# Kernel tuning notes

Hardware: AMD Instinct MI355X
Metric: run time of the kernel (lower is better)

## Reference

```python
import jax, jax.numpy as jnp
import numpy as np

BLOCK = 32  # GGML Q8_0 block size


def setup_inputs() -> dict:
    key = jax.random.key(0)
    k1, k2, k3, k4 = jax.random.split(key, 4)
    B, S, I, O = 2, 2048, 4096, 16384
    x = jax.random.normal(k1, (B, S, I), dtype=jnp.float32)
    # Q8_0-style signed 8-bit quants stored as int32 for portability
    qweight = jax.random.randint(k2, (O, I), -127, 128, dtype=jnp.int32)
    # one positive fp scale per 32-element block
    scales = jax.random.uniform(k3, (O, I // BLOCK), dtype=jnp.float32,
                                minval=0.005, maxval=0.02)
    bias = jax.random.normal(k4, (O,), dtype=jnp.float32) * 0.01
    return {"x": x, "qweight": qweight, "scales": scales, "bias": bias}


def reference(x, qweight, scales, bias):
    # dequantize_tensor: per-block scale * int8 quants -> full precision weight
    O, I = qweight.shape
    w = qweight.astype(x.dtype).reshape(O, I // BLOCK, BLOCK) * scales[:, :, None]
    w = w.reshape(O, I)  # [O, I]
    # Linear forward: y = x @ W^T + b
    return jnp.einsum('bsd,od->bso', x, w) + bias
```

## Files before the change

kernel.cpp:

```cpp
#include <hip/hip_runtime.h>
#include <cstdint>
#include <cstddef>

#define M_DIM 4096
#define N_DIM 16384
#define K_DIM 4096
#define QBLK 32

typedef __bf16 bf16x8 __attribute__((ext_vector_type(8)));
typedef float  f32x4  __attribute__((ext_vector_type(4)));
typedef unsigned short u16x8 __attribute__((ext_vector_type(8)));

__device__ __forceinline__ unsigned short f2bf(float f) {
    unsigned int x = __builtin_bit_cast(unsigned int, f);
    x += 0x7fffu + ((x >> 16) & 1u);
    return (unsigned short)(x >> 16);
}

__device__ __forceinline__ void gload16(const void* g, void* l) {
    __builtin_amdgcn_global_load_lds((__attribute__((address_space(1))) unsigned int*)(g),
                                     (__attribute__((address_space(3))) unsigned int*)(l),
                                     16, 0, 0);
}

__global__ __launch_bounds__(256) void cvt_x_kernel(const float* __restrict__ x,
                                                    unsigned short* __restrict__ o) {
    const size_t total = (size_t)M_DIM * K_DIM / 8;
    for (size_t i = (size_t)blockIdx.x * 256 + threadIdx.x; i < total;
         i += (size_t)gridDim.x * 256) {
        const float4* src = (const float4*)(x + i * 8);
        float4 a0 = src[0], a1 = src[1];
        u16x8 v;
        v[0] = f2bf(a0.x); v[1] = f2bf(a0.y); v[2] = f2bf(a0.z); v[3] = f2bf(a0.w);
        v[4] = f2bf(a1.x); v[5] = f2bf(a1.y); v[6] = f2bf(a1.z); v[7] = f2bf(a1.w);
        *(u16x8*)(o + i * 8) = v;
    }
}

__global__ __launch_bounds__(256) void dequant_w_kernel(const int* __restrict__ q,
                                                        const float* __restrict__ s,
                                                        unsigned short* __restrict__ o) {
    const size_t total = (size_t)N_DIM * K_DIM / 8;
    for (size_t i = (size_t)blockIdx.x * 256 + threadIdx.x; i < total;
         i += (size_t)gridDim.x * 256) {
        const int4* src = (const int4*)(q + i * 8);
        int4 q0 = src[0], q1 = src[1];
        float sc = s[i >> 2];
        u16x8 v;
        v[0] = f2bf((float)q0.x * sc); v[1] = f2bf((float)q0.y * sc);
        v[2] = f2bf((float)q0.z * sc); v[3] = f2bf((float)q0.w * sc);
        v[4] = f2bf((float)q1.x * sc); v[5] = f2bf((float)q1.y * sc);
        v[6] = f2bf((float)q1.z * sc); v[7] = f2bf((float)q1.w * sc);
        *(u16x8*)(o + i * 8) = v;
    }
}

__global__ __launch_bounds__(512, 2) void gemm256(
    const unsigned short* __restrict__ Abf, const unsigned short* __restrict__ Bbf,
    const float* __restrict__ bias, float* __restrict__ out) {

    __shared__ char smem[131072];

    const int t  = threadIdx.x;
    const int l  = t & 63;
    const int w  = t >> 6;
    const int wm = w >> 2;
    const int wn = w & 3;

    const int bid = blockIdx.y * 64 + blockIdx.x;
    const int wg  = (bid & 7) * 128 + (bid >> 3);
    const int bx  = wg & 63;
    const int by  = wg >> 6;
    const int tileM = by * 256;
    const int tileN = bx * 256;

    const int sr = w * 8 + (l >> 3);
    const int cs = (l & 7) ^ (l >> 3);
    const char* aP = (const char*)Abf + (size_t)(tileM + sr) * (K_DIM * 2) + cs * 16;
    const char* bP = (const char*)Bbf + (size_t)(tileN + sr) * (K_DIM * 2) + cs * 16;
    const int wq = w * 1024;

    const int lrow = l & 15, l47 = l >> 4;
    const int sw = lrow & 7;
    const unsigned c0 = (unsigned)((l47 ^ sw) * 16);
    const unsigned c1 = (unsigned)(((4 + l47) ^ sw) * 16);
    const unsigned offA0 = (unsigned)((wm * 64 + lrow) * 128) + c0;
    const unsigned offA1 = (unsigned)((wm * 64 + lrow) * 128) + c1;
    const unsigned offB0 = (unsigned)((wn * 32 + lrow) * 128) + c0;
    const unsigned offB1 = (unsigned)((wn * 32 + lrow) * 128) + c1;

    bf16x8 avr[4][2];
    bf16x8 bvr[2][2][2];
    f32x4  acc[2][4][2][2] = {};

#define ST_A(H, KT, DB) do { \
    const char* g_ = aP + (size_t)(H) * 1048576u + (unsigned)(KT) * 128u; \
    char* d_ = smem + (DB) * 65536 + (H) * 16384 + wq; \
    gload16(g_, d_); gload16(g_ + 524288, d_ + 8192); } while (0)

#define ST_B(H, KT, DB) do { \
    const char* g_ = bP + (size_t)(H) * 1048576u + (unsigned)(KT) * 128u; \
    char* d_ = smem + (DB) * 65536 + 32768 + (H) * 16384 + wq; \
    gload16(g_, d_); gload16(g_ + 8192 * 64, d_ + 8192); } while (0)

#define RD_A(DB, MH) do { \
    const char* b_ = smem + (DB) * 65536 + (MH) * 16384; \
    _Pragma("unroll") for (int mf_ = 0; mf_ < 4; ++mf_) { \
        avr[mf_][0] = *(const bf16x8*)(b_ + offA0 + mf_ * 2048); \
        avr[mf_][1] = *(const bf16x8*)(b_ + offA1 + mf_ * 2048); } } while (0)

#define RD_B(DB, NH) do { \
    const char* b_ = smem + (DB) * 65536 + 32768 + (NH) * 16384; \
    _Pragma("unroll") for (int nf_ = 0; nf_ < 2; ++nf_) { \
        bvr[NH][nf_][0] = *(const bf16x8*)(b_ + offB0 + nf_ * 2048); \
        bvr[NH][nf_][1] = *(const bf16x8*)(b_ + offB1 + nf_ * 2048); } } while (0)

#define MMQ(MH, NH) do { __builtin_amdgcn_s_setprio(1); \
    _Pragma("unroll") for (int mf_ = 0; mf_ < 4; ++mf_) \
    _Pragma("unroll") for (int nf_ = 0; nf_ < 2; ++nf_) \
    _Pragma("unroll") for (int kk_ = 0; kk_ < 2; ++kk_) \
        acc[MH][mf_][NH][nf_] = __builtin_amdgcn_mfma_f32_16x16x32_bf16( \
            avr[mf_][kk_], bvr[NH][nf_][kk_], acc[MH][mf_][NH][nf_], 0, 0, 0); \
    __builtin_amdgcn_s_setprio(0); } while (0)

#define BAR __builtin_amdgcn_s_barrier()
#define LGKM do { asm volatile("s_waitcnt lgkmcnt(0)" ::: "memory"); \
                  __builtin_amdgcn_sched_barrier(0); } while (0)
#define VMC(N) asm volatile("s_waitcnt vmcnt(" #N ")" ::: "memory")

    ST_A(0, 0, 0); ST_A(1, 0, 0); ST_B(0, 0, 0); ST_B(1, 0, 0);
    ST_A(0, 1, 1); ST_B(0, 1, 1);
    VMC(4); BAR;

    for (int i = 0; i < 32; ++i) {
        const int k0 = 2 * i;
        const int ka = (k0 + 1) & 63;
        const int kb = (k0 + 2) & 63;
        const int kc = (k0 + 3) & 63;
        RD_A(0, 0); RD_B(0, 0); ST_A(1, ka, 1); BAR; LGKM; MMQ(0, 0); BAR;
        RD_B(0, 1);             ST_B(1, ka, 1); BAR; LGKM; MMQ(0, 1); BAR;
        RD_A(0, 1);             ST_A(0, kb, 0); BAR; LGKM; MMQ(1, 0); BAR;
                                ST_B(0, kb, 0); BAR;       MMQ(1, 1); VMC(4); BAR;
        RD_A(1, 0); RD_B(1, 0); ST_A(1, kb, 0); BAR; LGKM; MMQ(0, 0); BAR;
        RD_B(1, 1);             ST_B(1, kb, 0); BAR; LGKM; MMQ(0, 1); BAR;
        RD_A(1, 1);             ST_A(0, kc, 1); BAR; LGKM; MMQ(1, 0); BAR;
                                ST_B(0, kc, 1); BAR;       MMQ(1, 1); VMC(4); BAR;
    }

    VMC(0);

    #pragma unroll
    for (int mh = 0; mh < 2; ++mh)
    #pragma unroll
    for (int nh = 0; nh < 2; ++nh)
    #pragma unroll
    for (int nf = 0; nf < 2; ++nf) {
        const int col = tileN + nh * 128 + wn * 32 + nf * 16 + lrow;
        const float bv = bias[col];
        #pragma unroll
        for (int mf = 0; mf < 4; ++mf) {
            const int row0 = tileM + mh * 128 + wm * 64 + mf * 16 + l47 * 4;
            f32x4 v = acc[mh][mf][nh][nf];
            #pragma unroll
            for (int j = 0; j < 4; ++j)
                out[(size_t)(row0 + j) * N_DIM + col] = v[j] + bv;
        }
    }
#undef ST_A
#undef ST_B
#undef RD_A
#undef RD_B
#undef MMQ
#undef BAR
#undef LGKM
#undef VMC
}

__global__ __launch_bounds__(256, 2) void gemm_fused(
    const float* __restrict__ Xf, const int* __restrict__ Qw, const float* __restrict__ Sc,
    const float* __restrict__ bias, float* __restrict__ out) {

    __shared__ char smem[2 * 32768];
    const int t = threadIdx.x;
    const int l = t & 63;
    const int w = t >> 6;
    const int wm = w >> 1, wn = w & 1;
    const int rowA0 = blockIdx.y * 128;
    const int colB0 = blockIdx.x * 128;

    const int lr = l >> 3;
    const int sXor = (l & 7) ^ lr;

    const float* aSrcF[4]; const int* bSrcQ[4]; const float* bSrcS[4];
    #pragma unroll
    for (int j = 0; j < 4; ++j) {
        int c = w * 4 + j;
        aSrcF[j] = Xf + (size_t)(rowA0 + c * 8 + lr) * K_DIM + sXor * 8;
        bSrcQ[j] = Qw + (size_t)(colB0 + c * 8 + lr) * K_DIM + sXor * 8;
        bSrcS[j] = Sc + (size_t)(colB0 + c * 8 + lr) * (K_DIM / QBLK) + (sXor >> 2);
    }

    const int lrow = l & 15, l47 = l >> 4, lx = l & 7;
    const unsigned raB0 = (unsigned)((wm * 64 + lrow) * 128 + ((l47 ^ lx) * 16));
    const unsigned raB1 = (unsigned)((wm * 64 + lrow) * 128 + (((4 | l47) ^ lx) * 16));
    const unsigned rbB0 = (unsigned)(16384 + (wn * 64 + lrow) * 128 + ((l47 ^ lx) * 16));
    const unsigned rbB1 = (unsigned)(16384 + (wn * 64 + lrow) * 128 + (((4 | l47) ^ lx) * 16));

    float fA[4][8]; int qB[4][8]; float sB[4];
    auto load_s = [&]() {
        #pragma unroll
        for (int j = 0; j < 4; ++j) {
            float4 a0 = ((const float4*)aSrcF[j])[0];
            float4 a1 = ((const float4*)aSrcF[j])[1];
            fA[j][0] = a0.x; fA[j][1] = a0.y; fA[j][2] = a0.z; fA[j][3] = a0.w;
            fA[j][4] = a1.x; fA[j][5] = a1.y; fA[j][6] = a1.z; fA[j][7] = a1.w;
            aSrcF[j] += 64;
            int4 b0 = ((const int4*)bSrcQ[j])[0];
            int4 b1 = ((const int4*)bSrcQ[j])[1];
            qB[j][0] = b0.x; qB[j][1] = b0.y; qB[j][2] = b0.z; qB[j][3] = b0.w;
            qB[j][4] = b1.x; qB[j][5] = b1.y; qB[j][6] = b1.z; qB[j][7] = b1.w;
            bSrcQ[j] += 64;
            sB[j] = *bSrcS[j]; bSrcS[j] += 2;
        }
    };
    auto write_s = [&](int bsel) {
        #pragma unroll
        for (int j = 0; j < 4; ++j) {
            u16x8 va, vb;
            #pragma unroll
            for (int e = 0; e < 8; ++e) va[e] = f2bf(fA[j][e]);
            #pragma unroll
            for (int e = 0; e < 8; ++e) vb[e] = f2bf((float)qB[j][e] * sB[j]);
            *(u16x8*)(&smem[bsel * 32768 + (w * 4 + j) * 1024 + l * 16]) = va;
            *(u16x8*)(&smem[bsel * 32768 + 16384 + (w * 4 + j) * 1024 + l * 16]) = vb;
        }
    };

    f32x4 acc[4][4] = {};
    load_s(); write_s(0);
    __syncthreads();
    int bsel = 0;
    for (int kt = 0; kt < 64; ++kt) {
        const bool pre = (kt + 1 < 64);
        if (pre) load_s();
        const unsigned boff = (unsigned)(bsel * 32768);
        #pragma unroll
        for (int kk = 0; kk < 2; ++kk) {
            bf16x8 av[4], bv[4];
            const unsigned ra = (kk ? raB1 : raB0) + boff;
            const unsigned rb = (kk ? rbB1 : rbB0) + boff;
            #pragma unroll
            for (int mf = 0; mf < 4; ++mf) av[mf] = *(const bf16x8*)(&smem[ra + mf * 2048]);
            #pragma unroll
            for (int nf = 0; nf < 4; ++nf) bv[nf] = *(const bf16x8*)(&smem[rb + nf * 2048]);
            #pragma unroll
            for (int mf = 0; mf < 4; ++mf)
                #pragma unroll
                for (int nf = 0; nf < 4; ++nf)
                    acc[mf][nf] = __builtin_amdgcn_mfma_f32_16x16x32_bf16(
                        av[mf], bv[nf], acc[mf][nf], 0, 0, 0);
        }
        if (pre) write_s(bsel ^ 1);
        __syncthreads();
        bsel ^= 1;
    }
    const int orow0 = rowA0 + wm * 64 + l47 * 4;
    const int ocol0 = colB0 + wn * 64 + lrow;
    #pragma unroll
    for (int nf = 0; nf < 4; ++nf) {
        const float bv = bias[ocol0 + nf * 16];
        #pragma unroll
        for (int mf = 0; mf < 4; ++mf) {
            f32x4 v = acc[mf][nf];
            #pragma unroll
            for (int j = 0; j < 4; ++j)
                out[(size_t)(orow0 + mf * 16 + j) * N_DIM + (ocol0 + nf * 16)] = v[j] + bv;
        }
    }
}

extern "C" void kernel_launch(void* const* d_in, const int* in_sizes, int n_in,
                              void* d_out, int out_size, void* d_ws, size_t ws_size,
                              hipStream_t stream) {
    const float* x    = (const float*)d_in[0];
    const int*   qw   = (const int*)d_in[1];
    const float* sc   = (const float*)d_in[2];
    const float* bias = (const float*)d_in[3];
    float* out = (float*)d_out;

    const size_t need = ((size_t)M_DIM * K_DIM + (size_t)N_DIM * K_DIM) * 2;
    if (ws_size >= need) {
        unsigned short* xb = (unsigned short*)d_ws;
        unsigned short* wb = xb + (size_t)M_DIM * K_DIM;
        cvt_x_kernel<<<dim3(2048), dim3(256), 0, stream>>>(x, xb);
        dequant_w_kernel<<<dim3(4096), dim3(256), 0, stream>>>(qw, sc, wb);
        gemm256<<<dim3(64, 16), dim3(512), 0, stream>>>(xb, wb, bias, out);
    } else {
        gemm_fused<<<dim3(128, 32), dim3(256), 0, stream>>>(x, qw, sc, bias, out);
    }
}
```

Measured before the change: 923.7 us.

## Issue all LDS fragment reads up front and drop intermediate barriers per k-tile

Restructures the 256x256 bf16 GEMM main loop so each k-tile loads all four A/B fragment sets from LDS at once into separate register buffers. MFMA groups are then gated by partial lgkmcnt waits instead of full waits. Three of the four block barriers per quarter-step are removed, leaving two per tile. The goal is less barrier and LDS-latency stall between MFMA bursts, at the cost of more live VGPRs (two A and two B fragment buffers) and a changed ordering of global-to-LDS stores relative to reads.

```diff
diff --git a/kernel.cpp b/kernel.cpp
--- a/kernel.cpp
+++ b/kernel.cpp
@@ -89,8 +89,8 @@
     const unsigned offB0 = (unsigned)((wn * 32 + lrow) * 128) + c0;
     const unsigned offB1 = (unsigned)((wn * 32 + lrow) * 128) + c1;
 
-    bf16x8 avr[4][2];
-    bf16x8 bvr[2][2][2];
+    bf16x8 avr0[4][2], avr1[4][2];
+    bf16x8 bvr0[2][2], bvr1[2][2];
     f32x4  acc[2][4][2][2] = {};
 
 #define ST_A(H, KT, DB) do { \
@@ -101,50 +101,55 @@
 #define ST_B(H, KT, DB) do { \
     const char* g_ = bP + (size_t)(H) * 1048576u + (unsigned)(KT) * 128u; \
     char* d_ = smem + (DB) * 65536 + 32768 + (H) * 16384 + wq; \
-    gload16(g_, d_); gload16(g_ + 8192 * 64, d_ + 8192); } while (0)
-
-#define RD_A(DB, MH) do { \
+    gload16(g_, d_); gload16(g_ + 524288, d_ + 8192); } while (0)
+
+#define RD_A(DB, MH, DST) do { \
     const char* b_ = smem + (DB) * 65536 + (MH) * 16384; \
     _Pragma("unroll") for (int mf_ = 0; mf_ < 4; ++mf_) { \
-        avr[mf_][0] = *(const bf16x8*)(b_ + offA0 + mf_ * 2048); \
-        avr[mf_][1] = *(const bf16x8*)(b_ + offA1 + mf_ * 2048); } } while (0)
-
-#define RD_B(DB, NH) do { \
+        DST[mf_][0] = *(const bf16x8*)(b_ + offA0 + mf_ * 2048); \
+        DST[mf_][1] = *(const bf16x8*)(b_ + offA1 + mf_ * 2048); } } while (0)
+
+#define RD_B(DB, NH, DST) do { \
     const char* b_ = smem + (DB) * 65536 + 32768 + (NH) * 16384; \
     _Pragma("unroll") for (int nf_ = 0; nf_ < 2; ++nf_) { \
-        bvr[NH][nf_][0] = *(const bf16x8*)(b_ + offB0 + nf_ * 2048); \
-        bvr[NH][nf_][1] = *(const bf16x8*)(b_ + offB1 + nf_ * 2048); } } while (0)
-
-#define MMQ(MH, NH) do { __builtin_amdgcn_s_setprio(1); \
+        DST[nf_][0] = *(const bf16x8*)(b_ + offB0 + nf_ * 2048); \
+        DST[nf_][1] = *(const bf16x8*)(b_ + offB1 + nf_ * 2048); } } while (0)
+
+#define MMQ(MH, NH, AV, BV) do { __builtin_amdgcn_s_setprio(1); \
     _Pragma("unroll") for (int mf_ = 0; mf_ < 4; ++mf_) \
     _Pragma("unroll") for (int nf_ = 0; nf_ < 2; ++nf_) \
     _Pragma("unroll") for (int kk_ = 0; kk_ < 2; ++kk_) \
         acc[MH][mf_][NH][nf_] = __builtin_amdgcn_mfma_f32_16x16x32_bf16( \
-            avr[mf_][kk_], bvr[NH][nf_][kk_], acc[MH][mf_][NH][nf_], 0, 0, 0); \
+            AV[mf_][kk_], BV[nf_][kk_], acc[MH][mf_][NH][nf_], 0, 0, 0); \
     __builtin_amdgcn_s_setprio(0); } while (0)
 
-#define BAR __builtin_amdgcn_s_barrier()
-#define LGKM do { asm volatile("s_waitcnt lgkmcnt(0)" ::: "memory"); \
-                  __builtin_amdgcn_sched_barrier(0); } while (0)
+#define BAR   __builtin_amdgcn_s_barrier()
+#define FENCE asm volatile("" ::: "memory")
+#define LGKM(N) do { asm volatile("s_waitcnt lgkmcnt(" #N ")" ::: "memory"); \
+                     __builtin_amdgcn_sched_barrier(0); } while (0)
 #define VMC(N) asm volatile("s_waitcnt vmcnt(" #N ")" ::: "memory")
 
-    ST_A(0, 0, 0); ST_A(1, 0, 0); ST_B(0, 0, 0); ST_B(1, 0, 0);
+    ST_A(0, 0, 0); ST_B(0, 0, 0); ST_A(1, 0, 0); ST_B(1, 0, 0);
     ST_A(0, 1, 1); ST_B(0, 1, 1);
     VMC(4); BAR;
 
+#define TILE(KT, DB) do { \
+    RD_A(DB, 0, avr0); RD_B(DB, 0, bvr0); FENCE; \
+    RD_A(DB, 1, avr1); FENCE; \
+    RD_B(DB, 1, bvr1); FENCE; \
+    ST_A(1, ((KT) + 1) & 63, (DB) ^ 1); ST_B(1, ((KT) + 1) & 63, (DB) ^ 1); \
+    LGKM(12); MMQ(0, 0, avr0, bvr0); \
+    LGKM(4);  MMQ(1, 0, avr1, bvr0); \
+    LGKM(0);  MMQ(0, 1, avr0, bvr1); \
+    BAR; \
+    ST_A(0, ((KT) + 2) & 63, DB); ST_B(0, ((KT) + 2) & 63, DB); \
+    MMQ(1, 1, avr1, bvr1); \
+    VMC(4); BAR; } while (0)
+
     for (int i = 0; i < 32; ++i) {
         const int k0 = 2 * i;
-        const int ka = (k0 + 1) & 63;
-        const int kb = (k0 + 2) & 63;
-        const int kc = (k0 + 3) & 63;
-        RD_A(0, 0); RD_B(0, 0); ST_A(1, ka, 1); BAR; LGKM; MMQ(0, 0); BAR;
-        RD_B(0, 1);             ST_B(1, ka, 1); BAR; LGKM; MMQ(0, 1); BAR;
-        RD_A(0, 1);             ST_A(0, kb, 0); BAR; LGKM; MMQ(1, 0); BAR;
-                                ST_B(0, kb, 0); BAR;       MMQ(1, 1); VMC(4); BAR;
-        RD_A(1, 0); RD_B(1, 0); ST_A(1, kb, 0); BAR; LGKM; MMQ(0, 0); BAR;
-        RD_B(1, 1);             ST_B(1, kb, 0); BAR; LGKM; MMQ(0, 1); BAR;
-        RD_A(1, 1);             ST_A(0, kc, 1); BAR; LGKM; MMQ(1, 0); BAR;
-                                ST_B(0, kc, 1); BAR;       MMQ(1, 1); VMC(4); BAR;
+        TILE(k0, 0);
+        TILE(k0 + 1, 1);
     }
 
     VMC(0);
@@ -172,8 +177,10 @@
 #undef RD_B
 #undef MMQ
 #undef BAR
+#undef FENCE
 #undef LGKM
 #undef VMC
+#undef TILE
 }
 
 __global__ __launch_bounds__(256, 2) void gemm_fused(
```

Result: no change. 930.8 us (+0.8%).
